# Performance work log

Measured on AMD Instinct MI355X. Metric: run time of the kernel, lower is better.

The kernel has to match this reference:

```python
import jax, jax.numpy as jnp
import numpy as np

B, F, ND, NE = 1024, 1024, 256, 256

def setup_inputs() -> dict:
    key = jax.random.key(0)
    k1, k2, k3 = jax.random.split(key, 3)
    x = jax.random.normal(k1, (B, F), dtype=jnp.float32)
    # xavier-uniform-like init scale for (F+1, units)
    lim_d = float(np.sqrt(6.0 / (F + 1 + ND)))
    lim_e = float(np.sqrt(6.0 / (F + 1 + NE)))
    dilations = jax.random.uniform(k2, (F + 1, ND), minval=-lim_d, maxval=lim_d, dtype=jnp.float32)
    erosions = jax.random.uniform(k3, (F + 1, NE), minval=-lim_e, maxval=lim_e, dtype=jnp.float32)
    return {"x": x, "dilations": dilations, "erosions": erosions}

def reference(x, dilations, erosions):
    b = x.shape[0]
    # append a zero 'bias' feature -> (b, F+1)
    xb = jnp.concatenate([x, jnp.zeros((b, 1), dtype=x.dtype)], axis=1)
    # tropical matmuls: max-plus (dilation), min-minus (erosion)
    dilated = jnp.max(xb[:, :, None] + dilations[None, :, :], axis=1)   # (b, ND)
    eroded = jnp.min(xb[:, :, None] - erosions[None, :, :], axis=1)     # (b, NE)
    return jnp.concatenate([eroded, dilated], axis=1)
```

## Files before the change

kernel.cpp:

```cpp
#include <hip/hip_runtime.h>
#include <math.h>

#define BB   1024
#define FF   1024
#define NOUT 512
#define NW   256
#define BT   128
#define CT   128
#define KS   16
#define KT   (FF / KS)
#define XT_OFF ((size_t)KS * BB * NOUT)

__global__ __launch_bounds__(256) void trop_transpose(
    const float* __restrict__ x, float* __restrict__ xt)
{
    __shared__ float t[64][65];
    const int f0 = blockIdx.x * 64;
    const int r0 = blockIdx.y * 64;
    const int tr = threadIdx.x >> 4;
    const int tc = threadIdx.x & 15;
#pragma unroll
    for (int q = 0; q < 4; ++q) {
        const int r = tr + q * 16;
        const float4 v = *(const float4*)(x + (size_t)(r0 + r) * FF + f0 + tc * 4);
        t[r][tc * 4 + 0] = v.x; t[r][tc * 4 + 1] = v.y;
        t[r][tc * 4 + 2] = v.z; t[r][tc * 4 + 3] = v.w;
    }
    __syncthreads();
#pragma unroll
    for (int q = 0; q < 4; ++q) {
        const int f = tr + q * 16;
        float4 v;
        v.x = t[tc * 4 + 0][f]; v.y = t[tc * 4 + 1][f];
        v.z = t[tc * 4 + 2][f]; v.w = t[tc * 4 + 3][f];
        *(float4*)(xt + (size_t)(f0 + f) * BB + r0 + tc * 4) = v;
    }
}

__global__ __launch_bounds__(256, 2) void trop_main(
    const float* __restrict__ xt,
    const float* __restrict__ dil,
    const float* __restrict__ ero,
    float* __restrict__ ws)
{
    const int bx = blockIdx.x;
    const int by = blockIdx.y;
    const int bz = blockIdx.z;
    const bool is_ero = (bx < 2);
    const float* __restrict__ w = is_ero ? ero : dil;
    const int c0w = (bx & 1) * CT;
    const int r0 = by * BT;

    const int tid = threadIdx.x;
    const int cg = tid & 15;
    const int rg = tid >> 4;

    float acc[8][8];
#pragma unroll
    for (int i = 0; i < 8; ++i)
#pragma unroll
        for (int j = 0; j < 8; ++j) acc[i][j] = -INFINITY;

    const float* xp = xt + (size_t)(bz * KT) * BB + r0 + rg * 8;
    const float* wp = w + (size_t)(bz * KT) * NW + c0w + cg * 4;

    if (is_ero) {
#pragma unroll 2
        for (int ff = 0; ff < KT; ff += 2) {
            const float4 xa0 = *(const float4*)(xp);
            const float4 xb0 = *(const float4*)(xp + 4);
            const float4 xa1 = *(const float4*)(xp + BB);
            const float4 xb1 = *(const float4*)(xp + BB + 4);
            const float4 wa0 = *(const float4*)(wp);
            const float4 wb0 = *(const float4*)(wp + 64);
            const float4 wa1 = *(const float4*)(wp + NW);
            const float4 wb1 = *(const float4*)(wp + NW + 64);
            xp += 2 * BB; wp += 2 * NW;
            const float xr0[8] = {xa0.x, xa0.y, xa0.z, xa0.w, xb0.x, xb0.y, xb0.z, xb0.w};
            const float xr1[8] = {xa1.x, xa1.y, xa1.z, xa1.w, xb1.x, xb1.y, xb1.z, xb1.w};
            const float wc0[8] = {wa0.x, wa0.y, wa0.z, wa0.w, wb0.x, wb0.y, wb0.z, wb0.w};
            const float wc1[8] = {wa1.x, wa1.y, wa1.z, wa1.w, wb1.x, wb1.y, wb1.z, wb1.w};
#pragma unroll
            for (int i = 0; i < 8; ++i)
#pragma unroll
                for (int j = 0; j < 8; ++j)
                    acc[i][j] = fmaxf(acc[i][j],
                                      fmaxf(wc0[j] - xr0[i], wc1[j] - xr1[i]));
        }
    } else {
#pragma unroll 2
        for (int ff = 0; ff < KT; ff += 2) {
            const float4 xa0 = *(const float4*)(xp);
            const float4 xb0 = *(const float4*)(xp + 4);
            const float4 xa1 = *(const float4*)(xp + BB);
            const float4 xb1 = *(const float4*)(xp + BB + 4);
            const float4 wa0 = *(const float4*)(wp);
            const float4 wb0 = *(const float4*)(wp + 64);
            const float4 wa1 = *(const float4*)(wp + NW);
            const float4 wb1 = *(const float4*)(wp + NW + 64);
            xp += 2 * BB; wp += 2 * NW;
            const float xr0[8] = {xa0.x, xa0.y, xa0.z, xa0.w, xb0.x, xb0.y, xb0.z, xb0.w};
            const float xr1[8] = {xa1.x, xa1.y, xa1.z, xa1.w, xb1.x, xb1.y, xb1.z, xb1.w};
            const float wc0[8] = {wa0.x, wa0.y, wa0.z, wa0.w, wb0.x, wb0.y, wb0.z, wb0.w};
            const float wc1[8] = {wa1.x, wa1.y, wa1.z, wa1.w, wb1.x, wb1.y, wb1.z, wb1.w};
#pragma unroll
            for (int i = 0; i < 8; ++i)
#pragma unroll
                for (int j = 0; j < 8; ++j)
                    acc[i][j] = fmaxf(acc[i][j],
                                      fmaxf(xr0[i] + wc0[j], xr1[i] + wc1[j]));
        }
    }

    if (bz == KS - 1) {
        const float4 ba = *(const float4*)(w + (size_t)FF * NW + c0w + cg * 4);
        const float4 bb = *(const float4*)(w + (size_t)FF * NW + c0w + 64 + cg * 4);
        const float bc[8] = {ba.x, ba.y, ba.z, ba.w, bb.x, bb.y, bb.z, bb.w};
#pragma unroll
        for (int i = 0; i < 8; ++i)
#pragma unroll
            for (int j = 0; j < 8; ++j) acc[i][j] = fmaxf(acc[i][j], bc[j]);
    }

    float* plane = ws + (size_t)bz * (BB * NOUT);
    const int cglob = bx * CT + cg * 4;
#pragma unroll
    for (int i = 0; i < 8; ++i) {
        const int row = r0 + rg * 8 + i;
        float4 v0, v1;
        v0.x = acc[i][0]; v0.y = acc[i][1]; v0.z = acc[i][2]; v0.w = acc[i][3];
        v1.x = acc[i][4]; v1.y = acc[i][5]; v1.z = acc[i][6]; v1.w = acc[i][7];
        *(float4*)(plane + (size_t)row * NOUT + cglob) = v0;
        *(float4*)(plane + (size_t)row * NOUT + cglob + 64) = v1;
    }
}

__global__ __launch_bounds__(256) void trop_combine(
    const float* __restrict__ ws, float* __restrict__ out)
{
    const int i4 = blockIdx.x * 256 + threadIdx.x;
    const float sgn = ((i4 & 127) < 64) ? -1.0f : 1.0f;
    const int stride4 = BB * NOUT / 4;
    float4 v = ((const float4*)ws)[i4];
#pragma unroll
    for (int z = 1; z < KS; ++z) {
        const float4 u = ((const float4*)ws)[(size_t)z * stride4 + i4];
        v.x = fmaxf(v.x, u.x); v.y = fmaxf(v.y, u.y);
        v.z = fmaxf(v.z, u.z); v.w = fmaxf(v.w, u.w);
    }
    v.x *= sgn; v.y *= sgn; v.z *= sgn; v.w *= sgn;
    ((float4*)out)[i4] = v;
}

extern "C" void kernel_launch(void* const* d_in, const int* in_sizes, int n_in,
                              void* d_out, int out_size, void* d_ws, size_t ws_size,
                              hipStream_t stream) {
    const float* x = (const float*)d_in[0];
    const float* dil = (const float*)d_in[1];
    const float* ero = (const float*)d_in[2];
    float* out = (float*)d_out;
    float* ws = (float*)d_ws;
    float* xt = ws + XT_OFF;

    dim3 tgrid(FF / 64, BB / 64);
    trop_transpose<<<tgrid, 256, 0, stream>>>(x, xt);

    dim3 grid(4, BB / BT, KS);
    trop_main<<<grid, 256, 0, stream>>>(xt, dil, ero, ws);

    trop_combine<<<BB * NOUT / 4 / 256, 256, 0, stream>>>(ws, out);
}
```

Measured before the change: 96.99 us.

## Stage x and weight tiles in LDS and double the K-split count

```diff
diff --git a/kernel.cpp b/kernel.cpp
--- a/kernel.cpp
+++ b/kernel.cpp
@@ -7,7 +7,7 @@
 #define NW   256
 #define BT   128
 #define CT   128
-#define KS   16
+#define KS   32
 #define KT   (FF / KS)
 #define XT_OFF ((size_t)KS * BB * NOUT)
 
@@ -37,7 +37,7 @@
     }
 }
 
-__global__ __launch_bounds__(256, 2) void trop_main(
+__global__ __launch_bounds__(256, 3) void trop_main(
     const float* __restrict__ xt,
     const float* __restrict__ dil,
     const float* __restrict__ ero,
@@ -50,10 +50,32 @@
     const float* __restrict__ w = is_ero ? ero : dil;
     const int c0w = (bx & 1) * CT;
     const int r0 = by * BT;
+    const int fb = bz * KT;
+
+    __shared__ float lds_x[KT][BT];
+    __shared__ float lds_w[KT][CT];
 
     const int tid = threadIdx.x;
     const int cg = tid & 15;
     const int rg = tid >> 4;
+
+#pragma unroll
+    for (int it = 0; it < 4; ++it) {
+        const int idx = it * 256 + tid;
+        const int f = idx >> 5;
+        const int r4 = idx & 31;
+        *(float4*)&lds_x[f][r4 * 4] =
+            *(const float4*)(xt + (size_t)(fb + f) * BB + r0 + r4 * 4);
+    }
+#pragma unroll
+    for (int it = 0; it < 4; ++it) {
+        const int idx = it * 256 + tid;
+        const int f = idx >> 5;
+        const int c4 = idx & 31;
+        *(float4*)&lds_w[f][c4 * 4] =
+            *(const float4*)(w + (size_t)(fb + f) * NW + c0w + c4 * 4);
+    }
+    __syncthreads();
 
     float acc[8][8];
 #pragma unroll
@@ -61,48 +83,28 @@
 #pragma unroll
         for (int j = 0; j < 8; ++j) acc[i][j] = -INFINITY;
 
-    const float* xp = xt + (size_t)(bz * KT) * BB + r0 + rg * 8;
-    const float* wp = w + (size_t)(bz * KT) * NW + c0w + cg * 4;
-
-    if (is_ero) {
 #pragma unroll 2
-        for (int ff = 0; ff < KT; ff += 2) {
-            const float4 xa0 = *(const float4*)(xp);
-            const float4 xb0 = *(const float4*)(xp + 4);
-            const float4 xa1 = *(const float4*)(xp + BB);
-            const float4 xb1 = *(const float4*)(xp + BB + 4);
-            const float4 wa0 = *(const float4*)(wp);
-            const float4 wb0 = *(const float4*)(wp + 64);
-            const float4 wa1 = *(const float4*)(wp + NW);
-            const float4 wb1 = *(const float4*)(wp + NW + 64);
-            xp += 2 * BB; wp += 2 * NW;
-            const float xr0[8] = {xa0.x, xa0.y, xa0.z, xa0.w, xb0.x, xb0.y, xb0.z, xb0.w};
-            const float xr1[8] = {xa1.x, xa1.y, xa1.z, xa1.w, xb1.x, xb1.y, xb1.z, xb1.w};
-            const float wc0[8] = {wa0.x, wa0.y, wa0.z, wa0.w, wb0.x, wb0.y, wb0.z, wb0.w};
-            const float wc1[8] = {wa1.x, wa1.y, wa1.z, wa1.w, wb1.x, wb1.y, wb1.z, wb1.w};
+    for (int ff = 0; ff < KT; ff += 2) {
+        const float4 xa0 = *(const float4*)&lds_x[ff][rg * 8];
+        const float4 xb0 = *(const float4*)&lds_x[ff][rg * 8 + 4];
+        const float4 xa1 = *(const float4*)&lds_x[ff + 1][rg * 8];
+        const float4 xb1 = *(const float4*)&lds_x[ff + 1][rg * 8 + 4];
+        const float4 wa0 = *(const float4*)&lds_w[ff][cg * 4];
+        const float4 wb0 = *(const float4*)&lds_w[ff][64 + cg * 4];
+        const float4 wa1 = *(const float4*)&lds_w[ff + 1][cg * 4];
+        const float4 wb1 = *(const float4*)&lds_w[ff + 1][64 + cg * 4];
+        const float xr0[8] = {xa0.x, xa0.y, xa0.z, xa0.w, xb0.x, xb0.y, xb0.z, xb0.w};
+        const float xr1[8] = {xa1.x, xa1.y, xa1.z, xa1.w, xb1.x, xb1.y, xb1.z, xb1.w};
+        const float wc0[8] = {wa0.x, wa0.y, wa0.z, wa0.w, wb0.x, wb0.y, wb0.z, wb0.w};
+        const float wc1[8] = {wa1.x, wa1.y, wa1.z, wa1.w, wb1.x, wb1.y, wb1.z, wb1.w};
+        if (is_ero) {
 #pragma unroll
             for (int i = 0; i < 8; ++i)
 #pragma unroll
                 for (int j = 0; j < 8; ++j)
                     acc[i][j] = fmaxf(acc[i][j],
                                       fmaxf(wc0[j] - xr0[i], wc1[j] - xr1[i]));
-        }
-    } else {
-#pragma unroll 2
-        for (int ff = 0; ff < KT; ff += 2) {
-            const float4 xa0 = *(const float4*)(xp);
-            const float4 xb0 = *(const float4*)(xp + 4);
-            const float4 xa1 = *(const float4*)(xp + BB);
-            const float4 xb1 = *(const float4*)(xp + BB + 4);
-            const float4 wa0 = *(const float4*)(wp);
-            const float4 wb0 = *(const float4*)(wp + 64);
-            const float4 wa1 = *(const float4*)(wp + NW);
-            const float4 wb1 = *(const float4*)(wp + NW + 64);
-            xp += 2 * BB; wp += 2 * NW;
-            const float xr0[8] = {xa0.x, xa0.y, xa0.z, xa0.w, xb0.x, xb0.y, xb0.z, xb0.w};
-            const float xr1[8] = {xa1.x, xa1.y, xa1.z, xa1.w, xb1.x, xb1.y, xb1.z, xb1.w};
-            const float wc0[8] = {wa0.x, wa0.y, wa0.z, wa0.w, wb0.x, wb0.y, wb0.z, wb0.w};
-            const float wc1[8] = {wa1.x, wa1.y, wa1.z, wa1.w, wb1.x, wb1.y, wb1.z, wb1.w};
+        } else {
 #pragma unroll
             for (int i = 0; i < 8; ++i)
 #pragma unroll
@@ -142,7 +144,7 @@
     const float sgn = ((i4 & 127) < 64) ? -1.0f : 1.0f;
     const int stride4 = BB * NOUT / 4;
     float4 v = ((const float4*)ws)[i4];
-#pragma unroll
+#pragma unroll 8
     for (int z = 1; z < KS; ++z) {
         const float4 u = ((const float4*)ws)[(size_t)z * stride4 + i4];
         v.x = fmaxf(v.x, u.x); v.y = fmaxf(v.y, u.y);
```

After: 95.64 us. About the same (-1.4%).
